# Optimization experiments

Hardware: AMD Instinct MI355X
Metric: run time of the kernel (lower is better)

The kernel has to match this reference:

```python
import jax, jax.numpy as jnp
import numpy as np
from jax import lax

# ---- model dims ----
NTOKEN = 60697
D_MODEL = 512
NLAYERS = 4
D_STATE = 16
D_CONV = 4
EXPAND = 2
D_INNER = EXPAND * D_MODEL      # 1024
DT_RANK = (D_MODEL + 15) // 16  # 32 (ceil(d_model/16), mamba default)
B_SZ = 4
SEQ = 2048
EPS = 1e-5


def setup_inputs() -> dict:
    key = jax.random.key(0)
    ks = jax.random.split(key, 16)
    s = 0.02
    src = jax.random.randint(ks[0], (B_SZ, SEQ), 0, NTOKEN)
    src_key_padding_mask = jnp.ones((B_SZ, SEQ), dtype=bool)
    emb_w = jax.random.normal(ks[1], (NTOKEN, D_MODEL), jnp.float32) * s
    enc_ln_w = jnp.ones((D_MODEL,), jnp.float32)
    enc_ln_b = jnp.zeros((D_MODEL,), jnp.float32)
    ln_w = jnp.ones((NLAYERS, D_MODEL), jnp.float32)
    ln_b = jnp.zeros((NLAYERS, D_MODEL), jnp.float32)
    in_proj_w = jax.random.normal(ks[2], (NLAYERS, 2 * D_INNER, D_MODEL), jnp.float32) * s
    conv_w = jax.random.normal(ks[3], (NLAYERS, D_INNER, D_CONV), jnp.float32) * 0.1
    conv_b = jnp.zeros((NLAYERS, D_INNER), jnp.float32)
    x_proj_w = jax.random.normal(ks[4], (NLAYERS, DT_RANK + 2 * D_STATE, D_INNER), jnp.float32) * s
    dt_proj_w = jax.random.normal(ks[5], (NLAYERS, D_INNER, DT_RANK), jnp.float32) * (DT_RANK ** -0.5)
    dt_proj_b = jax.random.uniform(ks[6], (NLAYERS, D_INNER), jnp.float32, -4.0, -2.0)
    # S4D real init: A = -[1..d_state], stored as log
    A_log = jnp.log(jnp.broadcast_to(jnp.arange(1, D_STATE + 1, dtype=jnp.float32),
                                     (NLAYERS, D_INNER, D_STATE)))
    D_skip = jnp.ones((NLAYERS, D_INNER), jnp.float32)
    out_proj_w = jax.random.normal(ks[7], (NLAYERS, D_MODEL, D_INNER), jnp.float32) * s / np.sqrt(NLAYERS)
    normf_w = jnp.ones((D_MODEL,), jnp.float32)
    normf_b = jnp.zeros((D_MODEL,), jnp.float32)
    return {
        'src': src, 'src_key_padding_mask': src_key_padding_mask,
        'emb_w': emb_w, 'enc_ln_w': enc_ln_w, 'enc_ln_b': enc_ln_b,
        'ln_w': ln_w, 'ln_b': ln_b, 'in_proj_w': in_proj_w,
        'conv_w': conv_w, 'conv_b': conv_b, 'x_proj_w': x_proj_w,
        'dt_proj_w': dt_proj_w, 'dt_proj_b': dt_proj_b,
        'A_log': A_log, 'D_skip': D_skip, 'out_proj_w': out_proj_w,
        'normf_w': normf_w, 'normf_b': normf_b,
    }


def _layer_norm(x, w, b, eps=EPS):
    mu = jnp.mean(x, axis=-1, keepdims=True)
    var = jnp.mean(jnp.square(x - mu), axis=-1, keepdims=True)
    return (x - mu) * lax.rsqrt(var + eps) * w + b


def _mamba_mixer(h, in_w, cw, cb, xw, dtw, dtb, A_log, D_skip, ow):
    B, L, _ = h.shape
    xz = h @ in_w.T                                   # [B,L,2*d_inner]
    x, z = jnp.split(xz, 2, axis=-1)
    # causal depthwise conv1d, kernel D_CONV
    xt = x.swapaxes(1, 2)                             # [B,d_inner,L]
    xp = jnp.pad(xt, ((0, 0), (0, 0), (D_CONV - 1, 0)))
    conv = cb[None, :, None]
    for k in range(D_CONV):
        conv = conv + cw[:, k][None, :, None] * xp[:, :, k:k + L]
    x = jax.nn.silu(conv).swapaxes(1, 2)              # [B,L,d_inner]
    xdbl = x @ xw.T                                   # [B,L,dt_rank+2*d_state]
    dt = jax.nn.softplus(xdbl[..., :DT_RANK] @ dtw.T + dtb)      # [B,L,d_inner]
    Bm = xdbl[..., DT_RANK:DT_RANK + D_STATE]                    # [B,L,d_state]
    Cm = xdbl[..., DT_RANK + D_STATE:]                           # [B,L,d_state]
    A = -jnp.exp(A_log)                               # [d_inner,d_state]

    def step(hst, inp):
        dt_t, b_t, c_t, x_t = inp                     # [B,d_inner],[B,d_state],[B,d_state],[B,d_inner]
        dA = jnp.exp(dt_t[..., None] * A)             # [B,d_inner,d_state]
        hst = dA * hst + (dt_t * x_t)[..., None] * b_t[:, None, :]
        y_t = jnp.einsum('bds,bs->bd', hst, c_t)
        return hst, y_t

    xs = (dt.swapaxes(0, 1), Bm.swapaxes(0, 1), Cm.swapaxes(0, 1), x.swapaxes(0, 1))
    h0 = jnp.zeros((B, D_INNER, D_STATE), dtype=h.dtype)
    _, ys = lax.scan(step, h0, xs)                    # ys: [L,B,d_inner]
    y = ys.swapaxes(0, 1) + x * D_skip
    y = y * jax.nn.silu(z)
    return y @ ow.T


def reference(src, src_key_padding_mask, emb_w, enc_ln_w, enc_ln_b, ln_w, ln_b,
              in_proj_w, conv_w, conv_b, x_proj_w, dt_proj_w, dt_proj_b,
              A_log, D_skip, out_proj_w, normf_w, normf_b):
    # GeneEncoder: embedding -> LayerNorm (dropout = identity in eval)
    hidden = _layer_norm(emb_w[src], enc_ln_w, enc_ln_b)
    residual = None
    for i in range(NLAYERS):  # prenorm Mamba Blocks
        residual = hidden if residual is None else hidden + residual
        hidden = _mamba_mixer(_layer_norm(residual, ln_w[i], ln_b[i]),
                              in_proj_w[i], conv_w[i], conv_b[i], x_proj_w[i],
                              dt_proj_w[i], dt_proj_b[i], A_log[i], D_skip[i],
                              out_proj_w[i])
    residual = hidden + residual
    return _layer_norm(residual, normf_w, normf_b)
```

## Files before the change

### kernel.cpp

```cpp
#include <hip/hip_runtime.h>
#include <hip/hip_bf16.h>
#include <math.h>

#define NTOKEN 60697
#define D_MODEL 512
#define NLAYERS 4
#define D_STATE 16
#define D_CONV 4
#define D_INNER 1024
#define DT_RANK 32
#define B_SZ 4
#define SEQ 2048
#define EPS 1e-5f
#define NROWS (B_SZ * SEQ)
#define CHUNK 128
#define NCHUNK (SEQ / CHUNK)
#define LOG2E 1.44269504f

typedef __bf16 bf16_t;
typedef __attribute__((ext_vector_type(8))) __bf16 bfx8;
typedef __attribute__((ext_vector_type(4))) __bf16 bfx4;
typedef __attribute__((ext_vector_type(4))) float f32x4;


__device__ __forceinline__ float fast_sigmoid(float x) {
    return 1.0f / (1.0f + __expf(-x));
}
__device__ __forceinline__ float silu(float x) {
    return x * fast_sigmoid(x);
}
__device__ __forceinline__ float softplus_f(float x) {
    return (x > 20.0f) ? x : log1pf(__expf(x));
}
__device__ __forceinline__ float exp2_fast(float x) {
    float r;
    asm("v_exp_f32 %0, %1" : "=v"(r) : "v"(x));
    return r;
}
__device__ __forceinline__ unsigned int bf16bits(float v) {
    return (unsigned int)__builtin_bit_cast(unsigned short, (bf16_t)v);
}
__device__ __forceinline__ float lo16f(unsigned int u) {
    return __builtin_bit_cast(float, u << 16);
}
__device__ __forceinline__ float hi16f(unsigned int u) {
    return __builtin_bit_cast(float, u & 0xFFFF0000u);
}

__device__ __forceinline__ void gload_lds16(const void* g, void* l) {
    __builtin_amdgcn_global_load_lds(
        (const __attribute__((address_space(1))) unsigned int*)g,
        (__attribute__((address_space(3))) unsigned int*)l, 16, 0, 0);
}

template <int CTRL>
__device__ __forceinline__ float dpp_fetch(float x) {
    int xi = __builtin_bit_cast(int, x);
    int yi = __builtin_amdgcn_update_dpp(0, xi, CTRL, 0xF, 0xF, true);
    return __builtin_bit_cast(float, yi);
}
__device__ __forceinline__ float dpp_sum16(float p) {
    p += dpp_fetch<0xB1>(p);
    p += dpp_fetch<0x4E>(p);
    p += dpp_fetch<0x141>(p);
    p += dpp_fetch<0x140>(p);
    return p;
}

__device__ __forceinline__ float blk_reduce_sum(float x, float* sbuf) {
#pragma unroll
    for (int m = 32; m >= 1; m >>= 1) x += __shfl_xor(x, m);
    int wid = threadIdx.x >> 6;
    if ((threadIdx.x & 63) == 0) sbuf[wid] = x;
    __syncthreads();
    float t = sbuf[0] + sbuf[1] + sbuf[2] + sbuf[3];
    __syncthreads();
    return t;
}

__global__ __launch_bounds__(256) void cast_bf16_kernel(
    const float* __restrict__ in, bf16_t* __restrict__ out, size_t n)
{
    size_t stride = (size_t)gridDim.x * 256 * 4;
    for (size_t i = ((size_t)blockIdx.x * 256 + threadIdx.x) * 4; i < n; i += stride) {
        float4 v = *reinterpret_cast<const float4*>(in + i);
        bfx4 o;
        o[0] = (bf16_t)v.x; o[1] = (bf16_t)v.y;
        o[2] = (bf16_t)v.z; o[3] = (bf16_t)v.w;
        *reinterpret_cast<bfx4*>(out + i) = o;
    }
}


__global__ __launch_bounds__(256) void embed_ln_kernel(
    const int* __restrict__ src, const float* __restrict__ emb,
    const float* __restrict__ w, const float* __restrict__ b,
    float* __restrict__ R)
{
    __shared__ float sbuf[4];
    int row = blockIdx.x;
    int tok = src[row];
    const float* e = emb + (size_t)tok * D_MODEL;
    int c0 = threadIdx.x, c1 = threadIdx.x + 256;
    float v0 = e[c0], v1 = e[c1];
    float mu = blk_reduce_sum(v0 + v1, sbuf) * (1.0f / D_MODEL);
    float d0 = v0 - mu, d1 = v1 - mu;
    float var = blk_reduce_sum(d0 * d0 + d1 * d1, sbuf) * (1.0f / D_MODEL);
    float rs = rsqrtf(var + EPS);
    size_t base = (size_t)row * D_MODEL;
    R[base + c0] = d0 * rs * w[c0] + b[c0];
    R[base + c1] = d1 * rs * w[c1] + b[c1];
}

__global__ __launch_bounds__(256) void add_ln_kernel(
    float* __restrict__ R, const float* __restrict__ Hadd,
    const float* __restrict__ w, const float* __restrict__ b,
    float* __restrict__ out, bf16_t* __restrict__ outb)
{
    __shared__ float sbuf[4];
    size_t base = (size_t)blockIdx.x * D_MODEL;
    int c0 = threadIdx.x, c1 = c0 + 256;
    float v0 = R[base + c0], v1 = R[base + c1];
    if (Hadd) {
        v0 += Hadd[base + c0];
        v1 += Hadd[base + c1];
        R[base + c0] = v0;
        R[base + c1] = v1;
    }
    float mu = blk_reduce_sum(v0 + v1, sbuf) * (1.0f / D_MODEL);
    float d0 = v0 - mu, d1 = v1 - mu;
    float var = blk_reduce_sum(d0 * d0 + d1 * d1, sbuf) * (1.0f / D_MODEL);
    float rs = rsqrtf(var + EPS);
    float o0 = d0 * rs * w[c0] + b[c0];
    float o1 = d1 * rs * w[c1] + b[c1];
    if (out) {
        out[base + c0] = o0;
        out[base + c1] = o1;
    }
    if (outb) {
        outb[base + c0] = (bf16_t)o0;
        outb[base + c1] = (bf16_t)o1;
    }
}

template <int EPI>
__global__ __launch_bounds__(256) void gemm_bf16_nt(
    const bf16_t* __restrict__ A, const bf16_t* __restrict__ B,
    float* __restrict__ C, int ldc, int K, const float* __restrict__ bias,
    const unsigned short* __restrict__ xcb_u16,
    unsigned int* __restrict__ dtx_u32,
    bf16_t* __restrict__ Cxb, bf16_t* __restrict__ Czb)
{
    __shared__ bf16_t As[128 * 32];
    __shared__ bf16_t Bs[128 * 32];
    int tid = threadIdx.x;
    int lane = tid & 63, wid = tid >> 6;
    int m0 = blockIdx.y * 128, n0 = blockIdx.x * 128;
    int wm = (wid >> 1) * 64, wn = (wid & 1) * 64;
    int c_lo = lane & 15;
    int khalf = lane >> 4;

    f32x4 acc[4][4];
#pragma unroll
    for (int i = 0; i < 4; i++)
#pragma unroll
        for (int j = 0; j < 4; j++)
            acc[i][j] = (f32x4){0.f, 0.f, 0.f, 0.f};

    for (int k0 = 0; k0 < K; k0 += 32) {
#pragma unroll
        for (int i = 0; i < 2; i++) {
            int c = i * 256 + tid;
            int row = c >> 2;
            int cb = (c & 3) * 16;
            int ldsoff = (i * 256 + wid * 64) * 16;
            gload_lds16((const char*)A + ((size_t)(m0 + row) * K + k0) * 2 + cb,
                        (char*)As + ldsoff);
            gload_lds16((const char*)B + ((size_t)(n0 + row) * K + k0) * 2 + cb,
                        (char*)Bs + ldsoff);
        }
        __syncthreads();

        bfx8 af[4], bfr[4];
#pragma unroll
        for (int i = 0; i < 4; i++) {
            af[i]  = *reinterpret_cast<const bfx8*>(As + (wm + i * 16 + c_lo) * 32 + khalf * 8);
            bfr[i] = *reinterpret_cast<const bfx8*>(Bs + (wn + i * 16 + c_lo) * 32 + khalf * 8);
        }
#pragma unroll
        for (int i = 0; i < 4; i++)
#pragma unroll
            for (int j = 0; j < 4; j++)
                acc[i][j] = __builtin_amdgcn_mfma_f32_16x16x32_bf16(af[i], bfr[j], acc[i][j], 0, 0, 0);
        __syncthreads();
    }

#pragma unroll
    for (int i = 0; i < 4; i++) {
#pragma unroll
        for (int j = 0; j < 4; j++) {
            int row0 = m0 + wm + i * 16 + khalf * 4;
            int col = n0 + wn + j * 16 + c_lo;
#pragma unroll
            for (int r = 0; r < 4; r++) {
                int row = row0 + r;
                float v = acc[i][j][r];
                if (EPI == 0) {
                    C[(size_t)row * ldc + col] = v;
                } else if (EPI == 2) {
                    v = softplus_f(v + bias[col]);
                    float xf = lo16f((unsigned int)xcb_u16[(size_t)row * D_INNER + col]);
                    unsigned int u = bf16bits(v) | (bf16bits(v * xf) << 16);
                    dtx_u32[(size_t)(row >> 1) * 2048 + col * 2 + (row & 1)] = u;
                } else if (EPI == 3) {
                    if (col < D_INNER) Cxb[(size_t)row * D_INNER + col] = (bf16_t)v;
                    else               Czb[(size_t)row * D_INNER + col - D_INNER] = (bf16_t)v;
                }
            }
        }
    }
}

__global__ __launch_bounds__(128) void gemm_xp_bf16(
    const bf16_t* __restrict__ A, const bf16_t* __restrict__ Bmat,
    bf16_t* __restrict__ XDlow, unsigned int* __restrict__ BCb, int K)
{
    __shared__ bf16_t As[64 * 32];
    __shared__ bf16_t Bs[64 * 32];
    int tid = threadIdx.x;
    int lane = tid & 63, w = tid >> 6;
    int m0 = blockIdx.x * 64;
    int wr0 = w * 32;
    int c_lo = lane & 15;
    int khalf = lane >> 4;

    f32x4 acc[2][4];
#pragma unroll
    for (int i = 0; i < 2; i++)
#pragma unroll
        for (int j = 0; j < 4; j++)
            acc[i][j] = (f32x4){0.f, 0.f, 0.f, 0.f};

    for (int k0 = 0; k0 < K; k0 += 32) {
#pragma unroll
        for (int call = 0; call < 2; call++) {
            int c = call * 128 + tid;
            int base = (call * 128 + w * 64) * 16;
            gload_lds16((const char*)A + ((size_t)(m0 + (c >> 2)) * K + k0) * 2 + (c & 3) * 16,
                        (char*)As + base);
            gload_lds16((const char*)Bmat + ((size_t)(c >> 2) * K + k0) * 2 + (c & 3) * 16,
                        (char*)Bs + base);
        }
        __syncthreads();

        bfx8 af[2], bfr[4];
#pragma unroll
        for (int i = 0; i < 2; i++)
            af[i] = *reinterpret_cast<const bfx8*>(As + (wr0 + i * 16 + c_lo) * 32 + khalf * 8);
#pragma unroll
        for (int j = 0; j < 4; j++)
            bfr[j] = *reinterpret_cast<const bfx8*>(Bs + (j * 16 + c_lo) * 32 + khalf * 8);
#pragma unroll
        for (int i = 0; i < 2; i++)
#pragma unroll
            for (int j = 0; j < 4; j++)
                acc[i][j] = __builtin_amdgcn_mfma_f32_16x16x32_bf16(af[i], bfr[j], acc[i][j], 0, 0, 0);
        __syncthreads();
    }

#pragma unroll
    for (int i = 0; i < 2; i++) {
        int row0 = m0 + wr0 + i * 16 + khalf * 4;
#pragma unroll
        for (int r = 0; r < 4; r++) {
            int row = row0 + r;
            XDlow[(size_t)row * DT_RANK + c_lo]      = (bf16_t)acc[i][0][r];
            XDlow[(size_t)row * DT_RANK + 16 + c_lo] = (bf16_t)acc[i][1][r];
            unsigned int u = bf16bits(acc[i][2][r]) | (bf16bits(acc[i][3][r]) << 16);
            BCb[(size_t)(row >> 1) * 32 + c_lo * 2 + (row & 1)] = u;
        }
    }
}

__global__ __launch_bounds__(256) void conv_silu_kernel(
    const bf16_t* __restrict__ Xrawb, const float* __restrict__ cw,
    const float* __restrict__ cb, bf16_t* __restrict__ XCb)
{
    size_t gid = (size_t)blockIdx.x * 256 + threadIdx.x;
    int d = (int)(gid & (D_INNER - 1));
    size_t bt = gid >> 10;
    int t = (int)(bt & (SEQ - 1));
    float acc = cb[d];
#pragma unroll
    for (int k = 0; k < D_CONV; k++) {
        int tt = t + k - (D_CONV - 1);
        if (tt >= 0)
            acc += cw[d * D_CONV + k] * (float)Xrawb[(bt + (size_t)(k - (D_CONV - 1))) * D_INNER + d];
    }
    XCb[gid] = (bf16_t)silu(acc);
}

__device__ __forceinline__ void scan_stage64(
    char* base, const unsigned int* __restrict__ DTXp,
    const unsigned int* __restrict__ BCp, size_t rowpair0, int d0, int tid)
{
    gload_lds16(DTXp + (rowpair0 + (size_t)(tid >> 3)) * 2048 + d0 * 2 + (tid & 7) * 4,
                base + tid * 16);
    gload_lds16(BCp + rowpair0 * 32 + tid * 4, base + 4096 + tid * 16);
}

__global__ __launch_bounds__(256) void scan_pA_kernel(
    const unsigned int* __restrict__ DTXb, const unsigned int* __restrict__ BCb,
    const float* __restrict__ A_log,
    float* __restrict__ DcB, float* __restrict__ UcB)
{
    __shared__ __align__(16) char lds[2][8192];
    const int tid = threadIdx.x;
    const int s = tid & 15, dl = tid >> 4;
    const int b = blockIdx.x >> 6;
    const int d0 = (blockIdx.x & 63) * 16;
    const int c = blockIdx.y;
    const int d = d0 + dl;
    const float Av2 = -__expf(A_log[d * D_STATE + s]) * LOG2E;
    const size_t bbase = (size_t)b * SEQ;
    const int tstart = c * CHUNK;

    float h = 0.f, cum = 0.f;
    scan_stage64(lds[0], DTXb, BCb, (bbase + tstart) >> 1, d0, tid);
    __syncthreads();
    int cur = 0;
    for (int t0 = 0; t0 < CHUNK; t0 += 64) {
        if (t0 + 64 < CHUNK)
            scan_stage64(lds[cur ^ 1], DTXb, BCb, (bbase + tstart + t0 + 64) >> 1, d0, tid);
        const char* L = lds[cur];
#pragma unroll
        for (int kk2 = 0; kk2 < 32; kk2++) {
            uint2 dp = *(const uint2*)(L + kk2 * 128 + dl * 8);
            uint2 bp = *(const uint2*)(L + 4096 + kk2 * 128 + s * 8);
#pragma unroll
            for (int j = 0; j < 2; j++) {
                unsigned int pk = j ? dp.y : dp.x;
                unsigned int bk = j ? bp.y : bp.x;
                float dtv = lo16f(pk);
                float ux  = hi16f(pk);
                float bv  = lo16f(bk);
                float e = exp2_fast(dtv * Av2);
                h = fmaf(e, h, ux * bv);
                cum += dtv;
            }
        }
        __syncthreads();
        cur ^= 1;
    }
    size_t cb64 = ((size_t)c * B_SZ + b) * D_INNER + d;
    UcB[cb64 * 16 + s] = h;
    if (s == 0) DcB[cb64] = cum;
}

__global__ __launch_bounds__(256) void scan_p2_kernel(
    const float* __restrict__ A_log, const float* __restrict__ DcB,
    const float* __restrict__ UcB, float* __restrict__ HcB)
{
    int tid = threadIdx.x;
    int s = tid & 15, dl = tid >> 4;
    int chain = blockIdx.x * 16 + dl;
    int b = chain >> 10, d = chain & 1023;
    float Av = -__expf(A_log[d * D_STATE + s]);
    float Hv = 0.f;
    for (int c = 0; c < NCHUNK; c++) {
        size_t base = ((size_t)c * B_SZ + b) * D_INNER + d;
        HcB[base * 16 + s] = Hv;
        Hv = __expf(Av * DcB[base]) * Hv + UcB[base * 16 + s];
    }
}

__global__ __launch_bounds__(256) void scan_pB_kernel(
    const unsigned int* __restrict__ DTXb, const unsigned int* __restrict__ BCb,
    const float* __restrict__ HcB, const float* __restrict__ A_log,
    const bf16_t* __restrict__ Zbufb, const float* __restrict__ Dskip,
    bf16_t* __restrict__ XCb)
{
    __shared__ __align__(16) char lds[2][8192];
    __shared__ float ytile[32][17];
    const int tid = threadIdx.x;
    const int s = tid & 15, dl = tid >> 4;
    const int b = blockIdx.x >> 6;
    const int d0 = (blockIdx.x & 63) * 16;
    const int c = blockIdx.y;
    const int d = d0 + dl;
    const float Av2 = -__expf(A_log[d * D_STATE + s]) * LOG2E;
    const size_t bbase = (size_t)b * SEQ;
    const int tstart = c * CHUNK;

    float h = HcB[(((size_t)c * B_SZ + b) * D_INNER + d) * 16 + s];

    const int tl  = tid >> 3;
    const int dlo = (tid * 2) & 15;
    const float dsk0 = Dskip[d0 + dlo];
    const float dsk1 = Dskip[d0 + dlo + 1];

    scan_stage64(lds[0], DTXb, BCb, (bbase + tstart) >> 1, d0, tid);
    __syncthreads();
    int cur = 0;
    for (int t0 = 0; t0 < CHUNK; t0 += 64) {
        if (t0 + 64 < CHUNK)
            scan_stage64(lds[cur ^ 1], DTXb, BCb, (bbase + tstart + t0 + 64) >> 1, d0, tid);
        const char* L = lds[cur];
#pragma unroll
        for (int g = 0; g < 2; g++) {
#pragma unroll
            for (int half = 0; half < 2; half++) {
                float yhold = 0.f;
#pragma unroll
                for (int k8 = 0; k8 < 8; k8++) {
                    int kk2 = g * 16 + half * 8 + k8;
                    uint2 dp = *(const uint2*)(L + kk2 * 128 + dl * 8);
                    uint2 bp = *(const uint2*)(L + 4096 + kk2 * 128 + s * 8);
#pragma unroll
                    for (int j = 0; j < 2; j++) {
                        unsigned int pk = j ? dp.y : dp.x;
                        unsigned int bk = j ? bp.y : bp.x;
                        float dtv = lo16f(pk);
                        float ux  = hi16f(pk);
                        float bv  = lo16f(bk);
                        float cv  = hi16f(bk);
                        float e = exp2_fast(dtv * Av2);
                        h = fmaf(e, h, ux * bv);
                        float p = dpp_sum16(h * cv);
                        if (s == k8 * 2 + j + half * 0) {  }
                        int k16 = k8 * 2 + j;
                        if (s == k16) yhold = p;
                    }
                }
                ytile[half * 16 + s][dl] = yhold;
            }
            __syncthreads();
            {
                int t = tstart + t0 + g * 32 + tl;
                size_t row = (bbase + t) * (size_t)D_INNER + d0 + dlo;
                float y0 = ytile[tl][dlo];
                float y1 = ytile[tl][dlo + 1];
                unsigned int xw = *(const unsigned int*)(XCb + row);
                unsigned int zw = *(const unsigned int*)(Zbufb + row);
                float g0 = (y0 + lo16f(xw) * dsk0) * silu(lo16f(zw));
                float g1 = (y1 + hi16f(xw) * dsk1) * silu(hi16f(zw));
                unsigned int o = bf16bits(g0) | (bf16bits(g1) << 16);
                *(unsigned int*)(XCb + row) = o;
            }
            __syncthreads();
        }
        cur ^= 1;
    }
}


extern "C" void kernel_launch(void* const* d_in, const int* in_sizes, int n_in,
                              void* d_out, int out_size, void* d_ws, size_t ws_size,
                              hipStream_t stream) {
    const int*   src       = (const int*)d_in[0];
    const float* emb_w     = (const float*)d_in[2];
    const float* enc_ln_w  = (const float*)d_in[3];
    const float* enc_ln_b  = (const float*)d_in[4];
    const float* ln_w      = (const float*)d_in[5];
    const float* ln_b      = (const float*)d_in[6];
    const float* in_proj_w = (const float*)d_in[7];
    const float* conv_w    = (const float*)d_in[8];
    const float* conv_b    = (const float*)d_in[9];
    const float* x_proj_w  = (const float*)d_in[10];
    const float* dt_proj_w = (const float*)d_in[11];
    const float* dt_proj_b = (const float*)d_in[12];
    const float* A_log     = (const float*)d_in[13];
    const float* D_skip    = (const float*)d_in[14];
    const float* out_proj_w= (const float*)d_in[15];
    const float* normf_w   = (const float*)d_in[16];
    const float* normf_b   = (const float*)d_in[17];
    float* out = (float*)d_out;

    float* R    = (float*)d_ws;
    float* H    = R    + (size_t)NROWS * D_MODEL;
    float* DcB  = H    + (size_t)NROWS * D_MODEL;
    float* UcB  = DcB  + (size_t)NCHUNK * B_SZ * D_INNER;
    float* HcB  = UcB  + (size_t)NCHUNK * B_SZ * D_INNER * D_STATE;
    unsigned int* BCb = (unsigned int*)(HcB + (size_t)NCHUNK * B_SZ * D_INNER * D_STATE);
    unsigned int* DTXb = BCb + (size_t)(NROWS / 2) * 32;
    bf16_t* Hb    = (bf16_t*)(DTXb + (size_t)(NROWS / 2) * 2048);
    bf16_t* Xrawb = Hb    + (size_t)NROWS * D_MODEL;
    bf16_t* Zbufb = Xrawb + (size_t)NROWS * D_INNER;
    bf16_t* XCb   = Zbufb + (size_t)NROWS * D_INNER;
    bf16_t* XDlow = XCb   + (size_t)NROWS * D_INNER;
    bf16_t* Wib   = XDlow + (size_t)NROWS * DT_RANK;
    bf16_t* Wob   = Wib   + (size_t)NLAYERS * 2 * D_INNER * D_MODEL;
    bf16_t* xpb   = Wob   + (size_t)NLAYERS * D_MODEL * D_INNER;
    bf16_t* dtwb  = xpb   + (size_t)NLAYERS * 64 * D_INNER;

    cast_bf16_kernel<<<2048, 256, 0, stream>>>(in_proj_w, Wib, (size_t)NLAYERS * 2 * D_INNER * D_MODEL);
    cast_bf16_kernel<<<2048, 256, 0, stream>>>(out_proj_w, Wob, (size_t)NLAYERS * D_MODEL * D_INNER);
    cast_bf16_kernel<<<256, 256, 0, stream>>>(x_proj_w, xpb, (size_t)NLAYERS * 64 * D_INNER);
    cast_bf16_kernel<<<128, 256, 0, stream>>>(dt_proj_w, dtwb, (size_t)NLAYERS * D_INNER * DT_RANK);

    embed_ln_kernel<<<NROWS, 256, 0, stream>>>(src, emb_w, enc_ln_w, enc_ln_b, R);

    for (int L = 0; L < NLAYERS; L++) {
        const float* AlogL = A_log + (size_t)L * D_INNER * D_STATE;

        add_ln_kernel<<<NROWS, 256, 0, stream>>>(
            R, (L == 0) ? nullptr : H, ln_w + L * D_MODEL, ln_b + L * D_MODEL,
            nullptr, Hb);

        gemm_bf16_nt<3><<<dim3(16, 64), 256, 0, stream>>>(
            Hb, Wib + (size_t)L * 2 * D_INNER * D_MODEL, nullptr, 0, D_MODEL,
            nullptr, nullptr, nullptr, Xrawb, Zbufb);

        conv_silu_kernel<<<(NROWS * D_INNER) / 256, 256, 0, stream>>>(
            Xrawb, conv_w + (size_t)L * D_INNER * D_CONV, conv_b + (size_t)L * D_INNER, XCb);

        gemm_xp_bf16<<<NROWS / 64, 128, 0, stream>>>(
            XCb, xpb + (size_t)L * 64 * D_INNER, XDlow, BCb, D_INNER);

        gemm_bf16_nt<2><<<dim3(8, 64), 256, 0, stream>>>(
            XDlow, dtwb + (size_t)L * D_INNER * DT_RANK, nullptr, 0, DT_RANK,
            dt_proj_b + (size_t)L * D_INNER, (const unsigned short*)XCb, DTXb,
            nullptr, nullptr);

        scan_pA_kernel<<<dim3(B_SZ * 64, NCHUNK), 256, 0, stream>>>(
            DTXb, BCb, AlogL, DcB, UcB);
        scan_p2_kernel<<<256, 256, 0, stream>>>(AlogL, DcB, UcB, HcB);
        scan_pB_kernel<<<dim3(B_SZ * 64, NCHUNK), 256, 0, stream>>>(
            DTXb, BCb, HcB, AlogL, Zbufb, D_skip + (size_t)L * D_INNER, XCb);

        gemm_bf16_nt<0><<<dim3(4, 64), 256, 0, stream>>>(
            XCb, Wob + (size_t)L * D_MODEL * D_INNER, H, D_MODEL, D_INNER,
            nullptr, nullptr, nullptr, nullptr, nullptr);
    }

    add_ln_kernel<<<NROWS, 256, 0, stream>>>(R, H, normf_w, normf_b, out, nullptr);
}
```

Before: 1.084 ms.

## Split-K x_proj GEMM, fold chunk-state pass into scan, retile out_proj, vectorize conv

Rewrites the x_proj GEMM as a split-K kernel over 16-row tiles, with each of four waves handling a quarter of K and reducing through LDS. This gives many more blocks. The separate chunk-carry scan kernel is removed: each scan_pB block recomputes its incoming state serially from the per-chunk decay and state buffers, and its first LDS stage load is issued before that loop. out_proj gets a dedicated 128x64-tile kernel so it launches twice as many blocks. The conv+SiLU kernel now processes two channels per thread with packed loads. The trade-offs are redundant carry recomputation in later chunks and extra LDS traffic for the split-K reduction.

```diff
diff --git a/kernel.cpp b/kernel.cpp
--- a/kernel.cpp
+++ b/kernel.cpp
@@ -146,7 +146,7 @@
 template <int EPI>
 __global__ __launch_bounds__(256) void gemm_bf16_nt(
     const bf16_t* __restrict__ A, const bf16_t* __restrict__ B,
-    float* __restrict__ C, int ldc, int K, const float* __restrict__ bias,
+    int K, const float* __restrict__ bias,
     const unsigned short* __restrict__ xcb_u16,
     unsigned int* __restrict__ dtx_u32,
     bf16_t* __restrict__ Cxb, bf16_t* __restrict__ Czb)
@@ -205,9 +205,7 @@
             for (int r = 0; r < 4; r++) {
                 int row = row0 + r;
                 float v = acc[i][j][r];
-                if (EPI == 0) {
-                    C[(size_t)row * ldc + col] = v;
-                } else if (EPI == 2) {
+                if (EPI == 2) {
                     v = softplus_f(v + bias[col]);
                     float xf = lo16f((unsigned int)xcb_u16[(size_t)row * D_INNER + col]);
                     unsigned int u = bf16bits(v) | (bf16bits(v * xf) << 16);
@@ -221,64 +219,129 @@
     }
 }
 
-__global__ __launch_bounds__(128) void gemm_xp_bf16(
-    const bf16_t* __restrict__ A, const bf16_t* __restrict__ Bmat,
-    bf16_t* __restrict__ XDlow, unsigned int* __restrict__ BCb, int K)
-{
-    __shared__ bf16_t As[64 * 32];
+__global__ __launch_bounds__(256) void gemm_out_bf16(
+    const bf16_t* __restrict__ A, const bf16_t* __restrict__ B,
+    float* __restrict__ C, int K)
+{
+    __shared__ bf16_t As[128 * 32];
     __shared__ bf16_t Bs[64 * 32];
     int tid = threadIdx.x;
-    int lane = tid & 63, w = tid >> 6;
-    int m0 = blockIdx.x * 64;
-    int wr0 = w * 32;
+    int lane = tid & 63, wid = tid >> 6;
+    int m0 = blockIdx.y * 128, n0 = blockIdx.x * 64;
+    int wm = (wid >> 1) * 64, wn = (wid & 1) * 32;
     int c_lo = lane & 15;
     int khalf = lane >> 4;
 
-    f32x4 acc[2][4];
-#pragma unroll
-    for (int i = 0; i < 2; i++)
-#pragma unroll
-        for (int j = 0; j < 4; j++)
+    f32x4 acc[4][2];
+#pragma unroll
+    for (int i = 0; i < 4; i++)
+#pragma unroll
+        for (int j = 0; j < 2; j++)
             acc[i][j] = (f32x4){0.f, 0.f, 0.f, 0.f};
 
     for (int k0 = 0; k0 < K; k0 += 32) {
 #pragma unroll
-        for (int call = 0; call < 2; call++) {
-            int c = call * 128 + tid;
-            int base = (call * 128 + w * 64) * 16;
+        for (int i = 0; i < 2; i++) {
+            int c = i * 256 + tid;
             gload_lds16((const char*)A + ((size_t)(m0 + (c >> 2)) * K + k0) * 2 + (c & 3) * 16,
-                        (char*)As + base);
+                        (char*)As + (i * 256 + wid * 64) * 16);
+        }
+        {
+            int c = tid;
+            gload_lds16((const char*)B + ((size_t)(n0 + (c >> 2)) * K + k0) * 2 + (c & 3) * 16,
+                        (char*)Bs + wid * 1024);
+        }
+        __syncthreads();
+
+        bfx8 af[4], bfr[2];
+#pragma unroll
+        for (int i = 0; i < 4; i++)
+            af[i] = *reinterpret_cast<const bfx8*>(As + (wm + i * 16 + c_lo) * 32 + khalf * 8);
+#pragma unroll
+        for (int j = 0; j < 2; j++)
+            bfr[j] = *reinterpret_cast<const bfx8*>(Bs + (wn + j * 16 + c_lo) * 32 + khalf * 8);
+#pragma unroll
+        for (int i = 0; i < 4; i++)
+#pragma unroll
+            for (int j = 0; j < 2; j++)
+                acc[i][j] = __builtin_amdgcn_mfma_f32_16x16x32_bf16(af[i], bfr[j], acc[i][j], 0, 0, 0);
+        __syncthreads();
+    }
+
+#pragma unroll
+    for (int i = 0; i < 4; i++)
+#pragma unroll
+        for (int j = 0; j < 2; j++) {
+            int row0 = m0 + wm + i * 16 + khalf * 4;
+            int col = n0 + wn + j * 16 + c_lo;
+#pragma unroll
+            for (int r = 0; r < 4; r++)
+                C[(size_t)(row0 + r) * D_MODEL + col] = acc[i][j][r];
+        }
+}
+
+__global__ __launch_bounds__(256) void gemm_xp_bf16(
+    const bf16_t* __restrict__ A, const bf16_t* __restrict__ Bmat,
+    bf16_t* __restrict__ XDlow, unsigned int* __restrict__ BCb)
+{
+    __shared__ bf16_t As[4][16 * 32];
+    __shared__ bf16_t Bs[4][64 * 32];
+    __shared__ float red[4][16 * 64];
+    const int tid = threadIdx.x;
+    const int lane = tid & 63, w = tid >> 6;
+    const int m0 = blockIdx.x * 16;
+    const int c_lo = lane & 15, khalf = lane >> 4;
+    const int K = D_INNER;
+
+    f32x4 acc[4];
+#pragma unroll
+    for (int j = 0; j < 4; j++) acc[j] = (f32x4){0.f, 0.f, 0.f, 0.f};
+
+    for (int kt = 0; kt < 8; kt++) {
+        int k0 = w * 256 + kt * 32;
+        gload_lds16((const char*)A + ((size_t)(m0 + (lane >> 2)) * K + k0) * 2 + (lane & 3) * 16,
+                    (char*)&As[w][0]);
+#pragma unroll
+        for (int i = 0; i < 4; i++) {
+            int c = i * 64 + lane;
             gload_lds16((const char*)Bmat + ((size_t)(c >> 2) * K + k0) * 2 + (c & 3) * 16,
-                        (char*)Bs + base);
-        }
-        __syncthreads();
-
-        bfx8 af[2], bfr[4];
-#pragma unroll
-        for (int i = 0; i < 2; i++)
-            af[i] = *reinterpret_cast<const bfx8*>(As + (wr0 + i * 16 + c_lo) * 32 + khalf * 8);
-#pragma unroll
-        for (int j = 0; j < 4; j++)
-            bfr[j] = *reinterpret_cast<const bfx8*>(Bs + (j * 16 + c_lo) * 32 + khalf * 8);
-#pragma unroll
-        for (int i = 0; i < 2; i++)
-#pragma unroll
-            for (int j = 0; j < 4; j++)
-                acc[i][j] = __builtin_amdgcn_mfma_f32_16x16x32_bf16(af[i], bfr[j], acc[i][j], 0, 0, 0);
-        __syncthreads();
-    }
-
-#pragma unroll
-    for (int i = 0; i < 2; i++) {
-        int row0 = m0 + wr0 + i * 16 + khalf * 4;
-#pragma unroll
-        for (int r = 0; r < 4; r++) {
-            int row = row0 + r;
-            XDlow[(size_t)row * DT_RANK + c_lo]      = (bf16_t)acc[i][0][r];
-            XDlow[(size_t)row * DT_RANK + 16 + c_lo] = (bf16_t)acc[i][1][r];
-            unsigned int u = bf16bits(acc[i][2][r]) | (bf16bits(acc[i][3][r]) << 16);
-            BCb[(size_t)(row >> 1) * 32 + c_lo * 2 + (row & 1)] = u;
-        }
+                        (char*)&Bs[w][0] + i * 1024);
+        }
+        __syncthreads();
+
+        bfx8 af = *reinterpret_cast<const bfx8*>(&As[w][0] + c_lo * 32 + khalf * 8);
+#pragma unroll
+        for (int j = 0; j < 4; j++) {
+            bfx8 bfr = *reinterpret_cast<const bfx8*>(&Bs[w][0] + (j * 16 + c_lo) * 32 + khalf * 8);
+            acc[j] = __builtin_amdgcn_mfma_f32_16x16x32_bf16(af, bfr, acc[j], 0, 0, 0);
+        }
+        __syncthreads();
+    }
+
+#pragma unroll
+    for (int j = 0; j < 4; j++)
+#pragma unroll
+        for (int r = 0; r < 4; r++)
+            red[w][(khalf * 4 + r) * 64 + j * 16 + c_lo] = acc[j][r];
+    __syncthreads();
+
+    {
+        int row = tid >> 4, cp = tid & 15;
+        float v0 = red[0][row * 64 + 2 * cp] + red[1][row * 64 + 2 * cp]
+                 + red[2][row * 64 + 2 * cp] + red[3][row * 64 + 2 * cp];
+        float v1 = red[0][row * 64 + 2 * cp + 1] + red[1][row * 64 + 2 * cp + 1]
+                 + red[2][row * 64 + 2 * cp + 1] + red[3][row * 64 + 2 * cp + 1];
+        unsigned int u = bf16bits(v0) | (bf16bits(v1) << 16);
+        *(unsigned int*)(XDlow + (size_t)(m0 + row) * DT_RANK + 2 * cp) = u;
+    }
+    {
+        int rp = tid >> 5, s = (tid >> 1) & 15, par = tid & 1;
+        int row = 2 * rp + par;
+        float Bv = red[0][row * 64 + 32 + s] + red[1][row * 64 + 32 + s]
+                 + red[2][row * 64 + 32 + s] + red[3][row * 64 + 32 + s];
+        float Cv = red[0][row * 64 + 48 + s] + red[1][row * 64 + 48 + s]
+                 + red[2][row * 64 + 48 + s] + red[3][row * 64 + 48 + s];
+        BCb[(size_t)((m0 >> 1) + rp) * 32 + s * 2 + par] = bf16bits(Bv) | (bf16bits(Cv) << 16);
     }
 }
 
@@ -287,17 +350,23 @@
     const float* __restrict__ cb, bf16_t* __restrict__ XCb)
 {
     size_t gid = (size_t)blockIdx.x * 256 + threadIdx.x;
-    int d = (int)(gid & (D_INNER - 1));
-    size_t bt = gid >> 10;
+    int dp = (int)(gid & 511);
+    size_t bt = gid >> 9;
     int t = (int)(bt & (SEQ - 1));
-    float acc = cb[d];
+    const unsigned int* Xu = (const unsigned int*)Xrawb;
+    int d0 = 2 * dp;
+    float a0 = cb[d0], a1 = cb[d0 + 1];
 #pragma unroll
     for (int k = 0; k < D_CONV; k++) {
         int tt = t + k - (D_CONV - 1);
-        if (tt >= 0)
-            acc += cw[d * D_CONV + k] * (float)Xrawb[(bt + (size_t)(k - (D_CONV - 1))) * D_INNER + d];
-    }
-    XCb[gid] = (bf16_t)silu(acc);
+        if (tt >= 0) {
+            unsigned int u = Xu[(bt + (size_t)(k - (D_CONV - 1))) * 512 + dp];
+            a0 += cw[d0 * D_CONV + k] * lo16f(u);
+            a1 += cw[(d0 + 1) * D_CONV + k] * hi16f(u);
+        }
+    }
+    unsigned int o = bf16bits(silu(a0)) | (bf16bits(silu(a1)) << 16);
+    ((unsigned int*)XCb)[gid] = o;
 }
 
 __device__ __forceinline__ void scan_stage64(
@@ -357,26 +426,10 @@
     if (s == 0) DcB[cb64] = cum;
 }
 
-__global__ __launch_bounds__(256) void scan_p2_kernel(
-    const float* __restrict__ A_log, const float* __restrict__ DcB,
-    const float* __restrict__ UcB, float* __restrict__ HcB)
-{
-    int tid = threadIdx.x;
-    int s = tid & 15, dl = tid >> 4;
-    int chain = blockIdx.x * 16 + dl;
-    int b = chain >> 10, d = chain & 1023;
-    float Av = -__expf(A_log[d * D_STATE + s]);
-    float Hv = 0.f;
-    for (int c = 0; c < NCHUNK; c++) {
-        size_t base = ((size_t)c * B_SZ + b) * D_INNER + d;
-        HcB[base * 16 + s] = Hv;
-        Hv = __expf(Av * DcB[base]) * Hv + UcB[base * 16 + s];
-    }
-}
-
 __global__ __launch_bounds__(256) void scan_pB_kernel(
     const unsigned int* __restrict__ DTXb, const unsigned int* __restrict__ BCb,
-    const float* __restrict__ HcB, const float* __restrict__ A_log,
+    const float* __restrict__ DcB, const float* __restrict__ UcB,
+    const float* __restrict__ A_log,
     const bf16_t* __restrict__ Zbufb, const float* __restrict__ Dskip,
     bf16_t* __restrict__ XCb)
 {
@@ -392,14 +445,19 @@
     const size_t bbase = (size_t)b * SEQ;
     const int tstart = c * CHUNK;
 
-    float h = HcB[(((size_t)c * B_SZ + b) * D_INNER + d) * 16 + s];
+    scan_stage64(lds[0], DTXb, BCb, (bbase + tstart) >> 1, d0, tid);
+
+    float h = 0.f;
+    for (int j = 0; j < c; j++) {
+        size_t base = ((size_t)j * B_SZ + b) * D_INNER + d;
+        h = exp2_fast(Av2 * DcB[base]) * h + UcB[base * 16 + s];
+    }
 
     const int tl  = tid >> 3;
     const int dlo = (tid * 2) & 15;
     const float dsk0 = Dskip[d0 + dlo];
     const float dsk1 = Dskip[d0 + dlo + 1];
 
-    scan_stage64(lds[0], DTXb, BCb, (bbase + tstart) >> 1, d0, tid);
     __syncthreads();
     int cur = 0;
     for (int t0 = 0; t0 < CHUNK; t0 += 64) {
@@ -427,7 +485,6 @@
                         float e = exp2_fast(dtv * Av2);
                         h = fmaf(e, h, ux * bv);
                         float p = dpp_sum16(h * cv);
-                        if (s == k8 * 2 + j + half * 0) {  }
                         int k16 = k8 * 2 + j;
                         if (s == k16) yhold = p;
                     }
@@ -480,8 +537,7 @@
     float* H    = R    + (size_t)NROWS * D_MODEL;
     float* DcB  = H    + (size_t)NROWS * D_MODEL;
     float* UcB  = DcB  + (size_t)NCHUNK * B_SZ * D_INNER;
-    float* HcB  = UcB  + (size_t)NCHUNK * B_SZ * D_INNER * D_STATE;
-    unsigned int* BCb = (unsigned int*)(HcB + (size_t)NCHUNK * B_SZ * D_INNER * D_STATE);
+    unsigned int* BCb = (unsigned int*)(UcB + (size_t)NCHUNK * B_SZ * D_INNER * D_STATE);
     unsigned int* DTXb = BCb + (size_t)(NROWS / 2) * 32;
     bf16_t* Hb    = (bf16_t*)(DTXb + (size_t)(NROWS / 2) * 2048);
     bf16_t* Xrawb = Hb    + (size_t)NROWS * D_MODEL;
@@ -508,29 +564,27 @@
             nullptr, Hb);
 
         gemm_bf16_nt<3><<<dim3(16, 64), 256, 0, stream>>>(
-            Hb, Wib + (size_t)L * 2 * D_INNER * D_MODEL, nullptr, 0, D_MODEL,
+            Hb, Wib + (size_t)L * 2 * D_INNER * D_MODEL, D_MODEL,
             nullptr, nullptr, nullptr, Xrawb, Zbufb);
 
-        conv_silu_kernel<<<(NROWS * D_INNER) / 256, 256, 0, stream>>>(
+        conv_silu_kernel<<<(NROWS * D_INNER / 2) / 256, 256, 0, stream>>>(
             Xrawb, conv_w + (size_t)L * D_INNER * D_CONV, conv_b + (size_t)L * D_INNER, XCb);
 
-        gemm_xp_bf16<<<NROWS / 64, 128, 0, stream>>>(
-            XCb, xpb + (size_t)L * 64 * D_INNER, XDlow, BCb, D_INNER);
+        gemm_xp_bf16<<<NROWS / 16, 256, 0, stream>>>(
+            XCb, xpb + (size_t)L * 64 * D_INNER, XDlow, BCb);
 
         gemm_bf16_nt<2><<<dim3(8, 64), 256, 0, stream>>>(
-            XDlow, dtwb + (size_t)L * D_INNER * DT_RANK, nullptr, 0, DT_RANK,
+            XDlow, dtwb + (size_t)L * D_INNER * DT_RANK, DT_RANK,
             dt_proj_b + (size_t)L * D_INNER, (const unsigned short*)XCb, DTXb,
             nullptr, nullptr);
 
         scan_pA_kernel<<<dim3(B_SZ * 64, NCHUNK), 256, 0, stream>>>(
             DTXb, BCb, AlogL, DcB, UcB);
-        scan_p2_kernel<<<256, 256, 0, stream>>>(AlogL, DcB, UcB, HcB);
         scan_pB_kernel<<<dim3(B_SZ * 64, NCHUNK), 256, 0, stream>>>(
-            DTXb, BCb, HcB, AlogL, Zbufb, D_skip + (size_t)L * D_INNER, XCb);
-
-        gemm_bf16_nt<0><<<dim3(4, 64), 256, 0, stream>>>(
-            XCb, Wob + (size_t)L * D_MODEL * D_INNER, H, D_MODEL, D_INNER,
-            nullptr, nullptr, nullptr, nullptr, nullptr);
+            DTXb, BCb, DcB, UcB, AlogL, Zbufb, D_skip + (size_t)L * D_INNER, XCb);
+
+        gemm_out_bf16<<<dim3(D_MODEL / 64, NROWS / 128), 256, 0, stream>>>(
+            XCb, Wob + (size_t)L * D_MODEL * D_INNER, H, D_INNER);
     }
 
     add_ln_kernel<<<NROWS, 256, 0, stream>>>(R, H, normf_w, normf_b, out, nullptr);
```

Measured after the change: 1.136 ms. 4.8% more time.

## Use transpose-reduce in scan output, vectorize conv, merge weight casts

Applied to the files above, without the earlier changes.

The scan's per-timestep 16-lane DPP reduction is replaced by a batched transpose-reduction over 16 timesteps. It uses DPP and ds_swizzle butterflies, so each lane ends up holding its own timestep's sum with fewer cross-lane ops. The depthwise conv kernel now handles two channels per thread with 32-bit loads and stores. The four weight-cast launches are merged into one kernel. The transpose-reduce keeps 16 partials live per lane, which raises register pressure, and the ds_swizzle ops go through the LDS unit.

```diff
diff --git a/kernel.cpp b/kernel.cpp
--- a/kernel.cpp
+++ b/kernel.cpp
@@ -59,12 +59,37 @@
     int yi = __builtin_amdgcn_update_dpp(0, xi, CTRL, 0xF, 0xF, true);
     return __builtin_bit_cast(float, yi);
 }
-__device__ __forceinline__ float dpp_sum16(float p) {
-    p += dpp_fetch<0xB1>(p);
-    p += dpp_fetch<0x4E>(p);
-    p += dpp_fetch<0x141>(p);
-    p += dpp_fetch<0x140>(p);
-    return p;
+template <int IMM>
+__device__ __forceinline__ float ds_swz(float x) {
+    int r = __builtin_amdgcn_ds_swizzle(__builtin_bit_cast(int, x), IMM);
+    return __builtin_bit_cast(float, r);
+}
+
+__device__ __forceinline__ float transpose_reduce16(const float* p, int s) {
+    float q[8];
+#pragma unroll
+    for (int m = 0; m < 8; m++) {
+        float mine  = (s & 1) ? p[2 * m + 1] : p[2 * m];
+        float other = (s & 1) ? p[2 * m]     : p[2 * m + 1];
+        q[m] = mine + dpp_fetch<0xB1>(other);
+    }
+    float r4[4];
+#pragma unroll
+    for (int m = 0; m < 4; m++) {
+        float mine  = (s & 2) ? q[2 * m + 1] : q[2 * m];
+        float other = (s & 2) ? q[2 * m]     : q[2 * m + 1];
+        r4[m] = mine + dpp_fetch<0x4E>(other);
+    }
+    float w[2];
+#pragma unroll
+    for (int m = 0; m < 2; m++) {
+        float mine  = (s & 4) ? r4[2 * m + 1] : r4[2 * m];
+        float other = (s & 4) ? r4[2 * m]     : r4[2 * m + 1];
+        w[m] = mine + ds_swz<0x101F>(other);
+    }
+    float mine  = (s & 8) ? w[1] : w[0];
+    float other = (s & 8) ? w[0] : w[1];
+    return mine + ds_swz<0x201F>(other);
 }
 
 __device__ __forceinline__ float blk_reduce_sum(float x, float* sbuf) {
@@ -78,16 +103,26 @@
     return t;
 }
 
-__global__ __launch_bounds__(256) void cast_bf16_kernel(
-    const float* __restrict__ in, bf16_t* __restrict__ out, size_t n)
-{
+__global__ __launch_bounds__(256) void cast_all_kernel(
+    const float* __restrict__ s0, const float* __restrict__ s1,
+    const float* __restrict__ s2, const float* __restrict__ s3,
+    bf16_t* __restrict__ d0, bf16_t* __restrict__ d1,
+    bf16_t* __restrict__ d2, bf16_t* __restrict__ d3,
+    size_t n0, size_t n1, size_t n2, size_t n3)
+{
+    size_t ntot = n0 + n1 + n2 + n3;
     size_t stride = (size_t)gridDim.x * 256 * 4;
-    for (size_t i = ((size_t)blockIdx.x * 256 + threadIdx.x) * 4; i < n; i += stride) {
-        float4 v = *reinterpret_cast<const float4*>(in + i);
+    for (size_t i = ((size_t)blockIdx.x * 256 + threadIdx.x) * 4; i < ntot; i += stride) {
+        const float* s; bf16_t* dst; size_t off = i;
+        if (off < n0) { s = s0; dst = d0; }
+        else if ((off -= n0) < n1) { s = s1; dst = d1; }
+        else if ((off -= n1) < n2) { s = s2; dst = d2; }
+        else { off -= n2; s = s3; dst = d3; }
+        float4 v = *reinterpret_cast<const float4*>(s + off);
         bfx4 o;
         o[0] = (bf16_t)v.x; o[1] = (bf16_t)v.y;
         o[2] = (bf16_t)v.z; o[3] = (bf16_t)v.w;
-        *reinterpret_cast<bfx4*>(out + i) = o;
+        *reinterpret_cast<bfx4*>(dst + off) = o;
     }
 }
 
@@ -287,17 +322,23 @@
     const float* __restrict__ cb, bf16_t* __restrict__ XCb)
 {
     size_t gid = (size_t)blockIdx.x * 256 + threadIdx.x;
-    int d = (int)(gid & (D_INNER - 1));
-    size_t bt = gid >> 10;
+    int dp = (int)(gid & 511);
+    size_t bt = gid >> 9;
     int t = (int)(bt & (SEQ - 1));
-    float acc = cb[d];
+    const unsigned int* Xu = (const unsigned int*)Xrawb;
+    int d0 = 2 * dp;
+    float a0 = cb[d0], a1 = cb[d0 + 1];
 #pragma unroll
     for (int k = 0; k < D_CONV; k++) {
         int tt = t + k - (D_CONV - 1);
-        if (tt >= 0)
-            acc += cw[d * D_CONV + k] * (float)Xrawb[(bt + (size_t)(k - (D_CONV - 1))) * D_INNER + d];
-    }
-    XCb[gid] = (bf16_t)silu(acc);
+        if (tt >= 0) {
+            unsigned int u = Xu[(bt + (size_t)(k - (D_CONV - 1))) * 512 + dp];
+            a0 += cw[d0 * D_CONV + k] * lo16f(u);
+            a1 += cw[(d0 + 1) * D_CONV + k] * hi16f(u);
+        }
+    }
+    unsigned int o = bf16bits(silu(a0)) | (bf16bits(silu(a1)) << 16);
+    ((unsigned int*)XCb)[gid] = o;
 }
 
 __device__ __forceinline__ void scan_stage64(
@@ -410,29 +451,26 @@
         for (int g = 0; g < 2; g++) {
 #pragma unroll
             for (int half = 0; half < 2; half++) {
-                float yhold = 0.f;
+                float p[16];
 #pragma unroll
                 for (int k8 = 0; k8 < 8; k8++) {
                     int kk2 = g * 16 + half * 8 + k8;
                     uint2 dp = *(const uint2*)(L + kk2 * 128 + dl * 8);
                     uint2 bp = *(const uint2*)(L + 4096 + kk2 * 128 + s * 8);
-#pragma unroll
-                    for (int j = 0; j < 2; j++) {
-                        unsigned int pk = j ? dp.y : dp.x;
-                        unsigned int bk = j ? bp.y : bp.x;
-                        float dtv = lo16f(pk);
-                        float ux  = hi16f(pk);
-                        float bv  = lo16f(bk);
-                        float cv  = hi16f(bk);
-                        float e = exp2_fast(dtv * Av2);
-                        h = fmaf(e, h, ux * bv);
-                        float p = dpp_sum16(h * cv);
-                        if (s == k8 * 2 + j + half * 0) {  }
-                        int k16 = k8 * 2 + j;
-                        if (s == k16) yhold = p;
+                    {
+                        float dtv = lo16f(dp.x), ux = hi16f(dp.x);
+                        float bv = lo16f(bp.x), cv = hi16f(bp.x);
+                        h = fmaf(exp2_fast(dtv * Av2), h, ux * bv);
+                        p[2 * k8] = h * cv;
+                    }
+                    {
+                        float dtv = lo16f(dp.y), ux = hi16f(dp.y);
+                        float bv = lo16f(bp.y), cv = hi16f(bp.y);
+                        h = fmaf(exp2_fast(dtv * Av2), h, ux * bv);
+                        p[2 * k8 + 1] = h * cv;
                     }
                 }
-                ytile[half * 16 + s][dl] = yhold;
+                ytile[half * 16 + s][dl] = transpose_reduce16(p, s);
             }
             __syncthreads();
             {
@@ -493,10 +531,13 @@
     bf16_t* xpb   = Wob   + (size_t)NLAYERS * D_MODEL * D_INNER;
     bf16_t* dtwb  = xpb   + (size_t)NLAYERS * 64 * D_INNER;
 
-    cast_bf16_kernel<<<2048, 256, 0, stream>>>(in_proj_w, Wib, (size_t)NLAYERS * 2 * D_INNER * D_MODEL);
-    cast_bf16_kernel<<<2048, 256, 0, stream>>>(out_proj_w, Wob, (size_t)NLAYERS * D_MODEL * D_INNER);
-    cast_bf16_kernel<<<256, 256, 0, stream>>>(x_proj_w, xpb, (size_t)NLAYERS * 64 * D_INNER);
-    cast_bf16_kernel<<<128, 256, 0, stream>>>(dt_proj_w, dtwb, (size_t)NLAYERS * D_INNER * DT_RANK);
+    cast_all_kernel<<<2048, 256, 0, stream>>>(
+        in_proj_w, out_proj_w, x_proj_w, dt_proj_w,
+        Wib, Wob, xpb, dtwb,
+        (size_t)NLAYERS * 2 * D_INNER * D_MODEL,
+        (size_t)NLAYERS * D_MODEL * D_INNER,
+        (size_t)NLAYERS * 64 * D_INNER,
+        (size_t)NLAYERS * D_INNER * DT_RANK);
 
     embed_ln_kernel<<<NROWS, 256, 0, stream>>>(src, emb_w, enc_ln_w, enc_ln_b, R);
 
@@ -511,7 +552,7 @@
             Hb, Wib + (size_t)L * 2 * D_INNER * D_MODEL, nullptr, 0, D_MODEL,
             nullptr, nullptr, nullptr, Xrawb, Zbufb);
 
-        conv_silu_kernel<<<(NROWS * D_INNER) / 256, 256, 0, stream>>>(
+        conv_silu_kernel<<<(NROWS * D_INNER / 2) / 256, 256, 0, stream>>>(
             Xrawb, conv_w + (size_t)L * D_INNER * D_CONV, conv_b + (size_t)L * D_INNER, XCb);
 
         gemm_xp_bf16<<<NROWS / 64, 128, 0, stream>>>(
```

Measured after the change: 1.133 ms. +4.5%, slower.
